# Optimization experiments

Hardware: AMD Instinct MI355X
Metric: run time of the kernel (lower is better)

## Reference

```python
import jax, jax.numpy as jnp
import numpy as np

T, N, D, H, L = 256, 128, 1024, 1024, 2  # seq len, batch, input, hidden, layers


def setup_inputs() -> dict:
    key = jax.random.key(0)
    ks = jax.random.split(key, 7)
    s = 1.0 / np.sqrt(H)  # PyTorch LSTMCell init: U(-1/sqrt(H), 1/sqrt(H))
    return {
        "x": jax.random.normal(ks[0], (T, N, D), jnp.float32),
        "h0": jax.random.normal(ks[1], (L, N, H), jnp.float32),
        "c0": jax.random.normal(ks[2], (L, N, H), jnp.float32),
        # stacked per-layer params (layer 0 input dim == H so shapes match)
        "W_ih": jax.random.uniform(ks[3], (L, 4 * H, D), jnp.float32, -s, s),
        "W_hh": jax.random.uniform(ks[4], (L, 4 * H, H), jnp.float32, -s, s),
        "b_ih": jax.random.uniform(ks[5], (L, 4 * H), jnp.float32, -s, s),
        "b_hh": jax.random.uniform(ks[6], (L, 4 * H), jnp.float32, -s, s),
    }


def _lstm_cell(x, h, c, Wih, Whh, b):
    # gates layout (PyTorch order): input, forget, cell(g), output
    gates = x @ Wih.T + h @ Whh.T + b  # [N, 4H]
    i, f, g, o = jnp.split(gates, 4, axis=-1)
    c_new = jax.nn.sigmoid(f) * c + jax.nn.sigmoid(i) * jnp.tanh(g)
    h_new = jax.nn.sigmoid(o) * jnp.tanh(c_new)
    return h_new, c_new


def reference(x, h0, c0, W_ih, W_hh, b_ih, b_hh):
    num_layers = h0.shape[0]
    b = b_ih + b_hh  # [L, 4H]

    def step(carry, x_t):
        h, c = carry  # each [L, N, H]
        inp = x_t
        hs, cs = [], []
        for l in range(num_layers):  # small fixed layer count
            h_l, c_l = _lstm_cell(inp, h[l], c[l], W_ih[l], W_hh[l], b[l])
            hs.append(h_l)
            cs.append(c_l)
            inp = h_l  # mirrors x[t] = h[i] feeding the next layer
        return (jnp.stack(hs), jnp.stack(cs)), None

    (h, c), _ = jax.lax.scan(step, (h0, c0), x)
    return h[-1]  # [N, H] last layer hidden at final timestep
```

## Files before the change

kernel.cpp:

```cpp
#include <hip/hip_runtime.h>


typedef _Float16 f16;
typedef f16  v8f16 __attribute__((ext_vector_type(8)));
typedef float v4f32 __attribute__((ext_vector_type(4)));

#define TSTEPS 256
#define SLOT   131072u
static constexpr size_t HS_BANK = (size_t)258 * SLOT;

#define SZ_W     ((size_t)2*4096*2048*2)
#define SZ_B     ((size_t)2*4096*4)
#define SZ_HSEQ  ((size_t)2*258*SLOT*2)
#define SZ_BAR   ((size_t)4096)
#define SZ_XF    ((size_t)256*128*1024*2)
#define NEED1    (SZ_W + SZ_B + SZ_HSEQ + SZ_BAR)
#define NEED2    (NEED1 + SZ_XF)

__global__ void lstm_init(const float* __restrict__ x,
                          const float* __restrict__ h0,
                          const float* __restrict__ Wih, const float* __restrict__ Whh,
                          const float* __restrict__ bih, const float* __restrict__ bhh,
                          f16* __restrict__ wsW, float* __restrict__ wsB,
                          f16* __restrict__ hseq, unsigned* __restrict__ bar,
                          f16* __restrict__ xf, int do_xf)
{
    size_t tid  = (size_t)blockIdx.x * blockDim.x + threadIdx.x;
    size_t nthr = (size_t)gridDim.x * blockDim.x;
    for (size_t i = tid; i < 16777216u; i += nthr) {
        unsigned l = (unsigned)(i >> 23), rem = (unsigned)(i & 8388607u);
        unsigned col = rem >> 11, k = rem & 2047u;
        float v = (k < 1024u) ? Wih[(size_t)l*4194304u + (size_t)col*1024u + k]
                              : Whh[(size_t)l*4194304u + (size_t)col*1024u + (k-1024u)];
        wsW[i] = (f16)v;
    }
    for (size_t i = tid; i < 8192u; i += nthr) wsB[i] = bih[i] + bhh[i];
    for (size_t i = tid; i < 131072u; i += nthr) {
        unsigned n = (unsigned)(i >> 10), k = (unsigned)(i & 1023u);
        unsigned dst = ((k >> 3) << 10) + (n << 3) + (k & 7u);
        hseq[dst]           = (f16)h0[i];
        hseq[HS_BANK + dst] = (f16)h0[131072u + i];
    }
    for (size_t i = tid; i < 1024u; i += nthr) bar[i] = 0u;
    if (do_xf) {
        for (size_t i = tid; i < 33554432u; i += nthr) xf[i] = (f16)x[i];
    }
}

__device__ __forceinline__ float sigmoid_fast(float v) { return 1.0f / (1.0f + __expf(-v)); }
__device__ __forceinline__ float tanh_fast(float v)    { return 1.0f - 2.0f / (__expf(2.0f*v) + 1.0f); }

__device__ __forceinline__ v8f16 cvt8(v4f32 lo, v4f32 hi) {
    v8f16 r;
    r[0]=(f16)lo[0]; r[1]=(f16)lo[1]; r[2]=(f16)lo[2]; r[3]=(f16)lo[3];
    r[4]=(f16)hi[0]; r[5]=(f16)hi[1]; r[6]=(f16)hi[2]; r[7]=(f16)hi[3];
    return r;
}

__device__ __forceinline__ unsigned ld_cnt(const unsigned* p) {
    return __hip_atomic_load(p, __ATOMIC_RELAXED, __HIP_MEMORY_SCOPE_AGENT);
}

#define CHUNK 8

__device__ __forceinline__ void load_row(const f16* p, int off,
                                         v8f16 a0[CHUNK], v8f16 a1[CHUNK])
{
    #pragma unroll
    for (int i = 0; i < CHUNK; ++i) {
        a0[i] = *(const v8f16*)(p + off + 32*i);
        a1[i] = *(const v8f16*)(p + off + 16384 + 32*i);
    }
}

__device__ __forceinline__ void load_sm(const f16* p, int off,
                                        v8f16 a0[CHUNK], v8f16 a1[CHUNK])
{
    #pragma unroll
    for (int i = 0; i < CHUNK; ++i) {
        a0[i] = *(const v8f16*)(p + off + 4096*i);
        a1[i] = *(const v8f16*)(p + off + 128 + 4096*i);
    }
}

__device__ __forceinline__ void mfma_chunk(const v8f16 a0[CHUNK], const v8f16 a1[CHUNK],
                                           const f16 (*wl)[2056], int l15, int kq, int kbase,
                                           v4f32 acc[2][2])
{
    #pragma unroll
    for (int i = 0; i < CHUNK; ++i) {
        int k = kbase + 32*i;
        v8f16 b0 = *(const v8f16*)(&wl[l15     ][k + kq]);
        v8f16 b1 = *(const v8f16*)(&wl[16 + l15][k + kq]);
        acc[0][0] = __builtin_amdgcn_mfma_f32_16x16x32_f16(a0[i], b0, acc[0][0], 0, 0, 0);
        acc[0][1] = __builtin_amdgcn_mfma_f32_16x16x32_f16(a0[i], b1, acc[0][1], 0, 0, 0);
        acc[1][0] = __builtin_amdgcn_mfma_f32_16x16x32_f16(a1[i], b0, acc[1][0], 0, 0, 0);
        acc[1][1] = __builtin_amdgcn_mfma_f32_16x16x32_f16(a1[i], b1, acc[1][1], 0, 0, 0);
    }
}

__device__ __forceinline__ void reduce_splits(v4f32 acc[2][2], float (*gl)[36],
                                              int rb, int quad, int l15, int ks)
{
    if (ks == 0) {
        #pragma unroll
        for (int mt = 0; mt < 2; ++mt) {
            int rrow = (rb << 5) + (mt << 4) + (quad << 2);
            #pragma unroll
            for (int r = 0; r < 4; ++r) {
                gl[rrow + r][l15     ] = acc[mt][0][r];
                gl[rrow + r][16 + l15] = acc[mt][1][r];
            }
        }
    }
    __syncthreads();
    if (ks == 1) {
        #pragma unroll
        for (int mt = 0; mt < 2; ++mt) {
            int rrow = (rb << 5) + (mt << 4) + (quad << 2);
            #pragma unroll
            for (int r = 0; r < 4; ++r) {
                gl[rrow + r][l15     ] += acc[mt][0][r];
                gl[rrow + r][16 + l15] += acc[mt][1][r];
            }
        }
    }
    __syncthreads();
}

__device__ __forceinline__ void cell2(const float (*gl)[36], int n1, int u,
                                      float bi, float bf, float bg, float bo,
                                      float& cr0, float& cr1, float& h0o, float& h1o)
{
    {
        float gi = gl[n1][u]      + bi;
        float gf = gl[n1][8 + u]  + bf;
        float gg = gl[n1][16 + u] + bg;
        float go = gl[n1][24 + u] + bo;
        float cn = sigmoid_fast(gf) * cr0 + sigmoid_fast(gi) * tanh_fast(gg);
        cr0 = cn;
        h0o = sigmoid_fast(go) * tanh_fast(cn);
    }
    {
        int n = n1 + 64;
        float gi = gl[n][u]      + bi;
        float gf = gl[n][8 + u]  + bf;
        float gg = gl[n][16 + u] + bg;
        float go = gl[n][24 + u] + bo;
        float cn = sigmoid_fast(gf) * cr1 + sigmoid_fast(gi) * tanh_fast(gg);
        cr1 = cn;
        h1o = sigmoid_fast(go) * tanh_fast(cn);
    }
}

__device__ __forceinline__ void store_h_slot(f16 (*hst)[8], f16* slotbase, int s,
                                             int tid, int n1, int u,
                                             float hv0, float hv1)
{
    hst[n1     ][u] = (f16)hv0;
    hst[n1 + 64][u] = (f16)hv1;
    __syncthreads();
    if (tid < 128) {
        union { v8f16 v; unsigned long long q[2]; } c;
        c.v = *(const v8f16*)&hst[tid][0];
        unsigned long long* gp = (unsigned long long*)(slotbase + ((size_t)s << 10) + (tid << 3));
        __hip_atomic_store(gp,     c.q[0], __ATOMIC_RELAXED, __HIP_MEMORY_SCOPE_AGENT);
        __hip_atomic_store(gp + 1, c.q[1], __ATOMIC_RELAXED, __HIP_MEMORY_SCOPE_AGENT);
    }
}

template<bool XF16>
__global__ void __launch_bounds__(512)
lstm_main(const float* __restrict__ x, const f16* __restrict__ xf,
          const f16* __restrict__ wsW, const float* __restrict__ wsB,
          f16* __restrict__ hseq, const float* __restrict__ c0,
          float* __restrict__ out, unsigned* __restrict__ bar)
{
    __shared__ f16   wlds[32][2056];
    __shared__ float glds[128][36];
    __shared__ f16   hst[128][8];

    const int tid   = threadIdx.x;
    const int wgid  = blockIdx.x;
    const int layer = wgid >> 7;
    const int s     = wgid & 127;
    const int lane  = tid & 63;
    const int wave  = tid >> 6;
    const int quad  = lane >> 4;
    const int l15   = lane & 15;
    const int rb    = wave & 3;
    const int ks    = wave >> 2;

    for (int idx = tid; idx < 8192; idx += 512) {
        int cc = idx >> 8;
        int k8 = (idx & 255) << 3;
        int col = ((cc >> 3) << 10) + (s << 3) + (cc & 7);
        *(v8f16*)(&wlds[cc][k8]) =
            *(const v8f16*)(wsW + (((size_t)(layer*4096 + col)) << 11) + k8);
    }

    const int u  = tid & 7;
    const int jg = (s << 3) + u;
    const float bi = wsB[layer*4096 +        jg];
    const float bf = wsB[layer*4096 + 1024 + jg];
    const float bg = wsB[layer*4096 + 2048 + jg];
    const float bo = wsB[layer*4096 + 3072 + jg];
    const int n1 = tid >> 3;
    float cr0 = c0[((size_t)layer << 17) + ((size_t)n1 << 10) + jg];
    float cr1 = c0[((size_t)layer << 17) + ((size_t)(n1 + 64) << 10) + jg];

    __syncthreads();

    const int kq   = quad << 3;
    const int row0 = (rb << 5) + l15;
    const int kslc = ks << 9;
    const int arow = (row0 << 10) + kslc + kq;
    const int jrow = (((kslc + kq) >> 3) << 10) + (row0 << 3);

    f16* h0b = hseq;
    f16* h1b = hseq + HS_BANK;
    unsigned* f0 = bar;
    unsigned* f1 = bar + 512;

    v8f16 A0[CHUNK], A1[CHUNK], C0[CHUNK], C1[CHUNK];

    if (layer == 0) {
        for (int t = 0; t < TSTEPS; ++t) {
            v4f32 acc[2][2] = {};

            if (XF16) {
                const f16* xp = xf + ((size_t)t << 17) + arow;
                load_row(xp, 0,   A0, A1);
                load_row(xp, 256, C0, C1);
                __builtin_amdgcn_sched_barrier(0);
                mfma_chunk(A0, A1, wlds, l15, kq, kslc,       acc);
                mfma_chunk(C0, C1, wlds, l15, kq, kslc + 256, acc);
            } else {
                const float* p0 = x + ((size_t)t << 17) + arow;
                const float* p1 = p0 + (16 << 10);
                #pragma unroll
                for (int k = 0; k < 512; k += 32) {
                    v4f32 w0 = *(const v4f32*)(p0 + k), w1 = *(const v4f32*)(p0 + k + 4);
                    v4f32 y0 = *(const v4f32*)(p1 + k), y1 = *(const v4f32*)(p1 + k + 4);
                    v8f16 a0 = cvt8(w0, w1);
                    v8f16 a1 = cvt8(y0, y1);
                    v8f16 b0 = *(const v8f16*)(&wlds[l15     ][kslc + k + kq]);
                    v8f16 b1 = *(const v8f16*)(&wlds[16 + l15][kslc + k + kq]);
                    acc[0][0] = __builtin_amdgcn_mfma_f32_16x16x32_f16(a0, b0, acc[0][0], 0, 0, 0);
                    acc[0][1] = __builtin_amdgcn_mfma_f32_16x16x32_f16(a0, b1, acc[0][1], 0, 0, 0);
                    acc[1][0] = __builtin_amdgcn_mfma_f32_16x16x32_f16(a1, b0, acc[1][0], 0, 0, 0);
                    acc[1][1] = __builtin_amdgcn_mfma_f32_16x16x32_f16(a1, b1, acc[1][1], 0, 0, 0);
                }
            }

            if (t > 0) {
                if (tid < 128) {
                    const unsigned* fp = f0 + (tid << 2);
                    unsigned need = (unsigned)t;
                    while (ld_cnt(fp) < need) __builtin_amdgcn_s_sleep(1);
                }
                __syncthreads();
            }

            {
                const f16* hp = h0b + (size_t)t * SLOT + jrow;
                load_sm(hp, 0,     A0, A1);
                load_sm(hp, 32768, C0, C1);
                __builtin_amdgcn_sched_barrier(0);
                mfma_chunk(A0, A1, wlds, l15, kq, 1024 + kslc,       acc);
                mfma_chunk(C0, C1, wlds, l15, kq, 1024 + kslc + 256, acc);
            }

            reduce_splits(acc, glds, rb, quad, l15, ks);

            float hv0, hv1;
            cell2(glds, n1, u, bi, bf, bg, bo, cr0, cr1, hv0, hv1);
            store_h_slot(hst, h0b + (size_t)(t + 1) * SLOT, s, tid, n1, u, hv0, hv1);

            __syncthreads();
            if (tid == 0)
                __hip_atomic_store(f0 + (s << 2), (unsigned)(t + 1),
                                   __ATOMIC_RELAXED, __HIP_MEMORY_SCOPE_AGENT);
        }
    } else {
        v8f16 D0[CHUNK], D1[CHUNK];
        for (int t = 0; t < TSTEPS; ++t) {
            if (tid < 128) {
                if (t > 0) {
                    const unsigned* fp = f1 + (tid << 2);
                    unsigned need = (unsigned)t;
                    while (ld_cnt(fp) < need) __builtin_amdgcn_s_sleep(1);
                }
            } else if (tid < 256) {
                const unsigned* fp = f0 + ((tid - 128) << 2);
                unsigned need = (unsigned)(t + 1);
                while (ld_cnt(fp) < need) __builtin_amdgcn_s_sleep(1);
            }
            __syncthreads();

            v4f32 acc[2][2] = {};
            const f16* pp = h1b + (size_t)t * SLOT + jrow;
            const f16* qp = h0b + (size_t)(t + 1) * SLOT + jrow;

            load_sm(pp, 0,     A0, A1);
            load_sm(pp, 32768, C0, C1);
            __builtin_amdgcn_sched_barrier(0);
            mfma_chunk(A0, A1, wlds, l15, kq, 1024 + kslc,       acc);
            load_sm(qp, 0,     D0, D1);
            mfma_chunk(C0, C1, wlds, l15, kq, 1024 + kslc + 256, acc);
            load_sm(qp, 32768, A0, A1);
            mfma_chunk(D0, D1, wlds, l15, kq, kslc,       acc);
            mfma_chunk(A0, A1, wlds, l15, kq, kslc + 256, acc);

            reduce_splits(acc, glds, rb, quad, l15, ks);

            float hv0, hv1;
            cell2(glds, n1, u, bi, bf, bg, bo, cr0, cr1, hv0, hv1);
            if (t < TSTEPS - 1) {
                store_h_slot(hst, h1b + (size_t)(t + 1) * SLOT, s, tid, n1, u, hv0, hv1);
                __syncthreads();
                if (tid == 0)
                    __hip_atomic_store(f1 + (s << 2), (unsigned)(t + 1),
                                       __ATOMIC_RELAXED, __HIP_MEMORY_SCOPE_AGENT);
            } else {
                out[(n1 << 10) + jg] = hv0;
                out[((n1 + 64) << 10) + jg] = hv1;
            }
        }
    }
}

extern "C" void kernel_launch(void* const* d_in, const int* in_sizes, int n_in,
                              void* d_out, int out_size, void* d_ws, size_t ws_size,
                              hipStream_t stream) {
    const float* x   = (const float*)d_in[0];
    const float* h0  = (const float*)d_in[1];
    const float* c0  = (const float*)d_in[2];
    const float* Wih = (const float*)d_in[3];
    const float* Whh = (const float*)d_in[4];
    const float* bih = (const float*)d_in[5];
    const float* bhh = (const float*)d_in[6];
    float* out = (float*)d_out;

    char* ws = (char*)d_ws;
    const bool xf16 = (ws_size >= NEED2);

    f16*      wsW  = (f16*)ws;
    float*    wsB  = (float*)(ws + SZ_W);
    f16*      hseq = (f16*)(ws + SZ_W + SZ_B);
    unsigned* bar  = (unsigned*)(ws + SZ_W + SZ_B + SZ_HSEQ);
    f16*      xf   = (f16*)(ws + NEED1);
    int do_xf = xf16 ? 1 : 0;

    lstm_init<<<2048, 256, 0, stream>>>(x, h0, Wih, Whh, bih, bhh,
                                        wsW, wsB, hseq, bar, xf, do_xf);

    void* kargs[] = { (void*)&x, (void*)&xf, (void*)&wsW, (void*)&wsB,
                      (void*)&hseq, (void*)&c0, (void*)&out, (void*)&bar };
    if (xf16) {
        hipLaunchCooperativeKernel((void*)&lstm_main<true>, dim3(256), dim3(512), kargs, 0, stream);
    } else {
        hipLaunchCooperativeKernel((void*)&lstm_main<false>, dim3(256), dim3(512), kargs, 0, stream);
    }
}
```

Baseline: 3.294 ms.

## Pack barrier flags densely and poll pairs with 64-bit loads

The per-block step counters are now packed contiguously instead of spaced 16 bytes apart. Each polling lane reads two counters at once with a 64-bit atomic load, so layer 1 can wait on both layers' flags from the same 64 threads. The sleep interval between polls is lengthened. The sched_barrier calls are replaced by empty asm statements that consume the loaded registers, so loads can overlap earlier MFMA chunks while the compiler still cannot reorder across them. Packing the flags together may add cache-line contention between writers.

```diff
diff --git a/kernel.cpp b/kernel.cpp
--- a/kernel.cpp
+++ b/kernel.cpp
@@ -57,11 +57,15 @@
     return r;
 }
 
-__device__ __forceinline__ unsigned ld_cnt(const unsigned* p) {
+__device__ __forceinline__ unsigned long long ld_pair(const unsigned long long* p) {
     return __hip_atomic_load(p, __ATOMIC_RELAXED, __HIP_MEMORY_SCOPE_AGENT);
 }
 
 #define CHUNK 8
+
+#define KA16(a0, a1) asm volatile("" :: \
+    "v"(a0[0]),"v"(a0[1]),"v"(a0[2]),"v"(a0[3]),"v"(a0[4]),"v"(a0[5]),"v"(a0[6]),"v"(a0[7]), \
+    "v"(a1[0]),"v"(a1[1]),"v"(a1[2]),"v"(a1[3]),"v"(a1[4]),"v"(a1[5]),"v"(a1[6]),"v"(a1[7]))
 
 __device__ __forceinline__ void load_row(const f16* p, int off,
                                          v8f16 a0[CHUNK], v8f16 a1[CHUNK])
@@ -220,7 +224,7 @@
     f16* h0b = hseq;
     f16* h1b = hseq + HS_BANK;
     unsigned* f0 = bar;
-    unsigned* f1 = bar + 512;
+    unsigned* f1 = bar + 128;
 
     v8f16 A0[CHUNK], A1[CHUNK], C0[CHUNK], C1[CHUNK];
 
@@ -232,8 +236,9 @@
                 const f16* xp = xf + ((size_t)t << 17) + arow;
                 load_row(xp, 0,   A0, A1);
                 load_row(xp, 256, C0, C1);
-                __builtin_amdgcn_sched_barrier(0);
+                KA16(A0, A1);
                 mfma_chunk(A0, A1, wlds, l15, kq, kslc,       acc);
+                KA16(C0, C1);
                 mfma_chunk(C0, C1, wlds, l15, kq, kslc + 256, acc);
             } else {
                 const float* p0 = x + ((size_t)t << 17) + arow;
@@ -254,10 +259,14 @@
             }
 
             if (t > 0) {
-                if (tid < 128) {
-                    const unsigned* fp = f0 + (tid << 2);
+                if (tid < 64) {
+                    const unsigned long long* fp = (const unsigned long long*)f0 + tid;
                     unsigned need = (unsigned)t;
-                    while (ld_cnt(fp) < need) __builtin_amdgcn_s_sleep(1);
+                    for (;;) {
+                        unsigned long long v = ld_pair(fp);
+                        if ((unsigned)v >= need && (unsigned)(v >> 32) >= need) break;
+                        __builtin_amdgcn_s_sleep(3);
+                    }
                 }
                 __syncthreads();
             }
@@ -266,8 +275,9 @@
                 const f16* hp = h0b + (size_t)t * SLOT + jrow;
                 load_sm(hp, 0,     A0, A1);
                 load_sm(hp, 32768, C0, C1);
-                __builtin_amdgcn_sched_barrier(0);
+                KA16(A0, A1);
                 mfma_chunk(A0, A1, wlds, l15, kq, 1024 + kslc,       acc);
+                KA16(C0, C1);
                 mfma_chunk(C0, C1, wlds, l15, kq, 1024 + kslc + 256, acc);
             }
 
@@ -279,22 +289,31 @@
 
             __syncthreads();
             if (tid == 0)
-                __hip_atomic_store(f0 + (s << 2), (unsigned)(t + 1),
+                __hip_atomic_store(f0 + s, (unsigned)(t + 1),
                                    __ATOMIC_RELAXED, __HIP_MEMORY_SCOPE_AGENT);
         }
     } else {
         v8f16 D0[CHUNK], D1[CHUNK];
         for (int t = 0; t < TSTEPS; ++t) {
-            if (tid < 128) {
+            if (tid < 64) {
                 if (t > 0) {
-                    const unsigned* fp = f1 + (tid << 2);
+                    const unsigned long long* fp = (const unsigned long long*)f1 + tid;
                     unsigned need = (unsigned)t;
-                    while (ld_cnt(fp) < need) __builtin_amdgcn_s_sleep(1);
+                    for (;;) {
+                        unsigned long long v = ld_pair(fp);
+                        if ((unsigned)v >= need && (unsigned)(v >> 32) >= need) break;
+                        __builtin_amdgcn_s_sleep(3);
+                    }
                 }
-            } else if (tid < 256) {
-                const unsigned* fp = f0 + ((tid - 128) << 2);
-                unsigned need = (unsigned)(t + 1);
-                while (ld_cnt(fp) < need) __builtin_amdgcn_s_sleep(1);
+                {
+                    const unsigned long long* fp = (const unsigned long long*)f0 + tid;
+                    unsigned need = (unsigned)(t + 1);
+                    for (;;) {
+                        unsigned long long v = ld_pair(fp);
+                        if ((unsigned)v >= need && (unsigned)(v >> 32) >= need) break;
+                        __builtin_amdgcn_s_sleep(3);
+                    }
+                }
             }
             __syncthreads();
 
@@ -304,12 +323,15 @@
 
             load_sm(pp, 0,     A0, A1);
             load_sm(pp, 32768, C0, C1);
-            __builtin_amdgcn_sched_barrier(0);
+            KA16(A0, A1);
             mfma_chunk(A0, A1, wlds, l15, kq, 1024 + kslc,       acc);
             load_sm(qp, 0,     D0, D1);
+            KA16(C0, C1);
             mfma_chunk(C0, C1, wlds, l15, kq, 1024 + kslc + 256, acc);
             load_sm(qp, 32768, A0, A1);
+            KA16(D0, D1);
             mfma_chunk(D0, D1, wlds, l15, kq, kslc,       acc);
+            KA16(A0, A1);
             mfma_chunk(A0, A1, wlds, l15, kq, kslc + 256, acc);
 
             reduce_splits(acc, glds, rb, quad, l15, ks);
@@ -320,7 +342,7 @@
                 store_h_slot(hst, h1b + (size_t)(t + 1) * SLOT, s, tid, n1, u, hv0, hv1);
                 __syncthreads();
                 if (tid == 0)
-                    __hip_atomic_store(f1 + (s << 2), (unsigned)(t + 1),
+                    __hip_atomic_store(f1 + s, (unsigned)(t + 1),
                                        __ATOMIC_RELAXED, __HIP_MEMORY_SCOPE_AGENT);
             } else {
                 out[(n1 << 10) + jg] = hv0;
```

Result: slower. 3.726 ms (+13.1%).

## Interleave layers across XCDs, split layer-0 flags, overlap layer-1 waits with loads

Applied to the files above, without the earlier changes.

Work-group to layer/slice mapping now interleaves by XCD, so each XCD hosts one layer's slices. Layer 0 publishes its progress flag to two separate arrays, one polled by layer 0 and one by layer 1, which reduces contention on shared flag lines. Layer 1 now waits for the layer-0 flag first, loads the layer-0 hidden state, then waits on its own recurrent flag, so that load overlaps the second wait. The cost is an extra atomic store per step and a longer sleep in the poll loops, which may add wake-up latency.

```diff
diff --git a/kernel.cpp b/kernel.cpp
--- a/kernel.cpp
+++ b/kernel.cpp
@@ -12,7 +12,7 @@
 #define SZ_W     ((size_t)2*4096*2048*2)
 #define SZ_B     ((size_t)2*4096*4)
 #define SZ_HSEQ  ((size_t)2*258*SLOT*2)
-#define SZ_BAR   ((size_t)4096)
+#define SZ_BAR   ((size_t)8192)
 #define SZ_XF    ((size_t)256*128*1024*2)
 #define NEED1    (SZ_W + SZ_B + SZ_HSEQ + SZ_BAR)
 #define NEED2    (NEED1 + SZ_XF)
@@ -41,7 +41,7 @@
         hseq[dst]           = (f16)h0[i];
         hseq[HS_BANK + dst] = (f16)h0[131072u + i];
     }
-    for (size_t i = tid; i < 1024u; i += nthr) bar[i] = 0u;
+    for (size_t i = tid; i < 2048u; i += nthr) bar[i] = 0u;
     if (do_xf) {
         for (size_t i = tid; i < 33554432u; i += nthr) xf[i] = (f16)x[i];
     }
@@ -181,9 +181,10 @@
     __shared__ f16   hst[128][8];
 
     const int tid   = threadIdx.x;
-    const int wgid  = blockIdx.x;
-    const int layer = wgid >> 7;
-    const int s     = wgid & 127;
+    const int bid   = blockIdx.x;
+    const int xcd   = bid & 7;
+    const int layer = (xcd >> 2);
+    const int s     = (bid >> 3) * 4 + (xcd & 3);
     const int lane  = tid & 63;
     const int wave  = tid >> 6;
     const int quad  = lane >> 4;
@@ -219,8 +220,9 @@
 
     f16* h0b = hseq;
     f16* h1b = hseq + HS_BANK;
-    unsigned* f0 = bar;
-    unsigned* f1 = bar + 512;
+    unsigned* f0a = bar;
+    unsigned* f0b = bar + 512;
+    unsigned* f1  = bar + 1024;
 
     v8f16 A0[CHUNK], A1[CHUNK], C0[CHUNK], C1[CHUNK];
 
@@ -255,7 +257,7 @@
 
             if (t > 0) {
                 if (tid < 128) {
-                    const unsigned* fp = f0 + (tid << 2);
+                    const unsigned* fp = f0a + (tid << 2);
                     unsigned need = (unsigned)t;
                     while (ld_cnt(fp) < need) __builtin_amdgcn_s_sleep(1);
                 }
@@ -278,39 +280,50 @@
             store_h_slot(hst, h0b + (size_t)(t + 1) * SLOT, s, tid, n1, u, hv0, hv1);
 
             __syncthreads();
-            if (tid == 0)
-                __hip_atomic_store(f0 + (s << 2), (unsigned)(t + 1),
+            if (tid == 0) {
+                __hip_atomic_store(f0a + (s << 2), (unsigned)(t + 1),
                                    __ATOMIC_RELAXED, __HIP_MEMORY_SCOPE_AGENT);
+                __hip_atomic_store(f0b + (s << 2), (unsigned)(t + 1),
+                                   __ATOMIC_RELAXED, __HIP_MEMORY_SCOPE_AGENT);
+            }
         }
     } else {
         v8f16 D0[CHUNK], D1[CHUNK];
         for (int t = 0; t < TSTEPS; ++t) {
-            if (tid < 128) {
-                if (t > 0) {
+            {
+                if (tid < 128) {
+                    const unsigned* fp = f0b + (tid << 2);
+                    unsigned need = (unsigned)(t + 1);
+                    while (ld_cnt(fp) < need) __builtin_amdgcn_s_sleep(2);
+                }
+                __syncthreads();
+            }
+
+            v4f32 acc[2][2] = {};
+            const f16* qp = h0b + (size_t)(t + 1) * SLOT + jrow;
+            const f16* pp = h1b + (size_t)t * SLOT + jrow;
+
+            load_sm(qp, 0,     A0, A1);
+            load_sm(qp, 32768, C0, C1);
+            __builtin_amdgcn_sched_barrier(0);
+
+            if (t > 0) {
+                if (tid < 128) {
                     const unsigned* fp = f1 + (tid << 2);
                     unsigned need = (unsigned)t;
-                    while (ld_cnt(fp) < need) __builtin_amdgcn_s_sleep(1);
+                    while (ld_cnt(fp) < need) __builtin_amdgcn_s_sleep(2);
                 }
-            } else if (tid < 256) {
-                const unsigned* fp = f0 + ((tid - 128) << 2);
-                unsigned need = (unsigned)(t + 1);
-                while (ld_cnt(fp) < need) __builtin_amdgcn_s_sleep(1);
             }
             __syncthreads();
 
-            v4f32 acc[2][2] = {};
-            const f16* pp = h1b + (size_t)t * SLOT + jrow;
-            const f16* qp = h0b + (size_t)(t + 1) * SLOT + jrow;
-
-            load_sm(pp, 0,     A0, A1);
-            load_sm(pp, 32768, C0, C1);
+            load_sm(pp, 0, D0, D1);
             __builtin_amdgcn_sched_barrier(0);
-            mfma_chunk(A0, A1, wlds, l15, kq, 1024 + kslc,       acc);
-            load_sm(qp, 0,     D0, D1);
-            mfma_chunk(C0, C1, wlds, l15, kq, 1024 + kslc + 256, acc);
-            load_sm(qp, 32768, A0, A1);
-            mfma_chunk(D0, D1, wlds, l15, kq, kslc,       acc);
-            mfma_chunk(A0, A1, wlds, l15, kq, kslc + 256, acc);
+            mfma_chunk(A0, A1, wlds, l15, kq, kslc,       acc);
+            load_sm(pp, 32768, A0, A1);
+            __builtin_amdgcn_sched_barrier(0);
+            mfma_chunk(C0, C1, wlds, l15, kq, kslc + 256, acc);
+            mfma_chunk(D0, D1, wlds, l15, kq, 1024 + kslc,       acc);
+            mfma_chunk(A0, A1, wlds, l15, kq, 1024 + kslc + 256, acc);
 
             reduce_splits(acc, glds, rb, quad, l15, ks);
 
```

Measured after the change: 3.139 ms. 1.05x faster.
